# Kernel tuning notes

Hardware: AMD Instinct MI355X
Metric: run time of the kernel (lower is better)

The kernel has to match this reference:

```python
import jax, jax.numpy as jnp
import numpy as np

NEG_SLOPE = 0.2


def setup_inputs() -> dict:
    key = jax.random.key(0)
    k1, k2, k3 = jax.random.split(key, 3)
    bs, n_agents, input_dim = 32, 512, 128
    n_heads, hidden_dim = 8, 64
    h = jax.random.normal(k1, (bs, n_agents, input_dim), dtype=jnp.float32)
    # Linear(input_dim, n_heads*hidden_dim, bias=False), stored as [in, out]
    W = jax.random.normal(k2, (input_dim, n_heads * hidden_dim), dtype=jnp.float32) * (1.0 / np.sqrt(input_dim))
    # xavier_uniform with gain=1.414 on shape (1, n_heads, 2*hidden_dim)
    fan = n_heads + 2 * hidden_dim
    bound = 1.414 * np.sqrt(6.0 / fan)
    att_a = jax.random.uniform(k3, (1, n_heads, 2 * hidden_dim), dtype=jnp.float32,
                               minval=-bound, maxval=bound)
    return {"h": h, "W": W, "att_a": att_a}


def reference(h, W, att_a):
    bs, n_agents, _ = h.shape
    n_heads = att_a.shape[1]
    hidden_dim = att_a.shape[2] // 2
    # h_prime: [bs, n_heads, n_agents, hidden_dim]
    h_prime = (h @ W).reshape(bs, n_agents, n_heads, hidden_dim).transpose(0, 2, 1, 3)
    # Additive score decomposes exactly: (a1.h_i + a2.h_j) == sum(cat(h_i,h_j)*a)
    a_src = att_a[0, :, :hidden_dim]   # [n_heads, hidden_dim]
    a_dst = att_a[0, :, hidden_dim:]   # [n_heads, hidden_dim]
    e_src = jnp.einsum('bhnd,hd->bhn', h_prime, a_src)  # score contribution of node i (row)
    e_dst = jnp.einsum('bhnd,hd->bhn', h_prime, a_dst)  # contribution of node j (col)
    e = e_src[:, :, :, None] + e_dst[:, :, None, :]     # [bs, n_heads, n, n]
    e = jnp.where(e >= 0, e, NEG_SLOPE * e)             # leaky_relu(0.2)
    attention = jax.nn.softmax(e, axis=-1)
    h_new = jnp.einsum('bhnm,bhmd->bhnd', attention, h_prime)
    return jax.nn.elu(h_new)
```

## Files before the change

kernel.cpp:

```cpp
#include <hip/hip_runtime.h>

#define BS 32
#define NA 512
#define ID 128
#define NH 8
#define HD 64
#define NHD 512
#define NEG 0.2f
#define NC 32
#define CH 16

__global__ __launch_bounds__(256) void k1_gemm(
    const float* __restrict__ h, const float* __restrict__ W,
    const float* __restrict__ att, float* __restrict__ hp,
    float* __restrict__ s_out, float* __restrict__ t_out) {
  int blk = blockIdx.x;
  int b = blk >> 5;
  int n0 = (blk & 31) * 16;
  int t = threadIdx.x;
  int lane = t & 63, w = t >> 6;
  int r0 = __builtin_amdgcn_readfirstlane((w >> 1) * 8);
  int chalf = __builtin_amdgcn_readfirstlane(w & 1);
  int col = chalf * 256 + lane * 4;
  int head = col >> 6;
  int d0 = col & 63;
  const float* arow = h + ((size_t)b * NA + n0 + r0) * ID;
  const float* wptr = W + col;

  float4 a0c = {0,0,0,0}, a1c = {0,0,0,0}, a2c = {0,0,0,0}, a3c = {0,0,0,0};
  float4 a4c = {0,0,0,0}, a5c = {0,0,0,0}, a6c = {0,0,0,0}, a7c = {0,0,0,0};

#define K1_ROW(I, C, KK)                                                      \
  { float a_ = arow[(I) * ID + kc + (KK)];                                    \
    C.x += a_ * wv.x; C.y += a_ * wv.y; C.z += a_ * wv.z; C.w += a_ * wv.w; }
  #pragma unroll 1
  for (int kc = 0; kc < ID; kc += 8) {
    #pragma unroll
    for (int kk = 0; kk < 8; ++kk) {
      float4 wv = *(const float4*)(wptr + (size_t)(kc + kk) * NHD);
      K1_ROW(0, a0c, kk) K1_ROW(1, a1c, kk) K1_ROW(2, a2c, kk)
      K1_ROW(3, a3c, kk) K1_ROW(4, a4c, kk) K1_ROW(5, a5c, kk)
      K1_ROW(6, a6c, kk) K1_ROW(7, a7c, kk)
    }
  }
#undef K1_ROW
  {
    size_t off = ((((size_t)b * NH + head) * NA) + (n0 + r0)) * HD + d0;
    *(float4*)(hp + off) = a0c; off += HD;
    *(float4*)(hp + off) = a1c; off += HD;
    *(float4*)(hp + off) = a2c; off += HD;
    *(float4*)(hp + off) = a3c; off += HD;
    *(float4*)(hp + off) = a4c; off += HD;
    *(float4*)(hp + off) = a5c; off += HD;
    *(float4*)(hp + off) = a6c; off += HD;
    *(float4*)(hp + off) = a7c;
  }
  {
    float4 as4 = *(const float4*)(att + head * 128 + d0);
    float4 ad4 = *(const float4*)(att + head * 128 + 64 + d0);
#define DOT4(C, A) ((C).x*(A).x + (C).y*(A).y + (C).z*(A).z + (C).w*(A).w)
    float sp0 = DOT4(a0c, as4), tp0 = DOT4(a0c, ad4);
    float sp1 = DOT4(a1c, as4), tp1 = DOT4(a1c, ad4);
    float sp2 = DOT4(a2c, as4), tp2 = DOT4(a2c, ad4);
    float sp3 = DOT4(a3c, as4), tp3 = DOT4(a3c, ad4);
    float sp4 = DOT4(a4c, as4), tp4 = DOT4(a4c, ad4);
    float sp5 = DOT4(a5c, as4), tp5 = DOT4(a5c, ad4);
    float sp6 = DOT4(a6c, as4), tp6 = DOT4(a6c, ad4);
    float sp7 = DOT4(a7c, as4), tp7 = DOT4(a7c, ad4);
#undef DOT4
    #pragma unroll
    for (int m = 1; m < 16; m <<= 1) {
      sp0 += __shfl_xor(sp0, m, 64); tp0 += __shfl_xor(tp0, m, 64);
      sp1 += __shfl_xor(sp1, m, 64); tp1 += __shfl_xor(tp1, m, 64);
      sp2 += __shfl_xor(sp2, m, 64); tp2 += __shfl_xor(tp2, m, 64);
      sp3 += __shfl_xor(sp3, m, 64); tp3 += __shfl_xor(tp3, m, 64);
      sp4 += __shfl_xor(sp4, m, 64); tp4 += __shfl_xor(tp4, m, 64);
      sp5 += __shfl_xor(sp5, m, 64); tp5 += __shfl_xor(tp5, m, 64);
      sp6 += __shfl_xor(sp6, m, 64); tp6 += __shfl_xor(tp6, m, 64);
      sp7 += __shfl_xor(sp7, m, 64); tp7 += __shfl_xor(tp7, m, 64);
    }
    int g16 = lane & 15;
    int rsel = g16 & 7;
    float sv_ = rsel == 0 ? sp0 : rsel == 1 ? sp1 : rsel == 2 ? sp2 :
                rsel == 3 ? sp3 : rsel == 4 ? sp4 : rsel == 5 ? sp5 :
                rsel == 6 ? sp6 : sp7;
    float tv_ = rsel == 0 ? tp0 : rsel == 1 ? tp1 : rsel == 2 ? tp2 :
                rsel == 3 ? tp3 : rsel == 4 ? tp4 : rsel == 5 ? tp5 :
                rsel == 6 ? tp6 : tp7;
    size_t off = (((size_t)b * NH + head) * NA) + n0 + r0 + rsel;
    if (g16 < 8) s_out[off] = sv_;
    else         t_out[off] = tv_;
  }
}

__global__ __launch_bounds__(512) void k2_fused(
    const float* __restrict__ hp, const float* __restrict__ s_g,
    const float* __restrict__ t_g, float* __restrict__ out) {
  __shared__ float tv[NA]; __shared__ int tpm[NA];
  __shared__ float sv[NA]; __shared__ int spm[NA];
  __shared__ float wp[NA]; __shared__ float wn[NA];
  __shared__ float localP[8 * 64]; __shared__ float localN[8 * 64];
  __shared__ float seedP[8 * 64];  __shared__ float seedN[8 * 64];
  __shared__ float totP[64];
  __shared__ float zps[NA + 1]; __shared__ float znp[NA + 1];
  __shared__ float szP[NC]; __shared__ float szN[NC];
  __shared__ float sufZ[NC + 1]; __shared__ float preZ[NC + 1];
  __shared__ float aA[NA]; __shared__ float aB[NA]; __shared__ float aI[NA];
  __shared__ int aJ[NA]; __shared__ int aR[NA];

  int bh = blockIdx.x;
  int t = threadIdx.x;
  int lane = t & 63, w = t >> 6;
  const float* vbase = hp + (size_t)bh * NA * HD;

  float tvr = t_g[(size_t)bh * NA + t]; int tir = t;
  float svr = s_g[(size_t)bh * NA + t]; int sir = t;
  for (int size = 2; size <= NA; size <<= 1) {
    bool dirAsc = ((t & size) == 0);
    for (int stride = size >> 1; stride > 0; stride >>= 1) {
      float ptv, psv; int pti, psi;
      if (stride >= 64) {
        tv[t] = tvr; tpm[t] = tir; sv[t] = svr; spm[t] = sir;
        __syncthreads();
        ptv = tv[t ^ stride]; pti = tpm[t ^ stride];
        psv = sv[t ^ stride]; psi = spm[t ^ stride];
        __syncthreads();
      } else {
        ptv = __shfl_xor(tvr, stride, 64); pti = __shfl_xor(tir, stride, 64);
        psv = __shfl_xor(svr, stride, 64); psi = __shfl_xor(sir, stride, 64);
      }
      bool mn = (((t & stride) == 0) == dirAsc);
      bool swt = mn ? (ptv < tvr) : (ptv > tvr);
      if (swt) { tvr = ptv; tir = pti; }
      bool sws = mn ? (psv > svr) : (psv < svr);
      if (sws) { svr = psv; sir = psi; }
    }
  }
  tv[t] = tvr; tpm[t] = tir; sv[t] = svr; spm[t] = sir;
  __syncthreads();

  float cmax = fmaxf(tv[NA - 1], 0.f);
  float amax = fmaxf(sv[0], 0.f);
  wp[t] = __expf(tv[t] - cmax);
  wn[t] = __expf(NEG * tv[t] - cmax);
  __syncthreads();

  if (t < 32) {
    float a = 0.f;
    for (int j = t * CH; j < t * CH + CH; ++j) a += wp[j];
    szP[t] = a;
  } else if (t < 64) {
    int c = t - 32; float a = 0.f;
    for (int j = c * CH; j < c * CH + CH; ++j) a += wn[j];
    szN[c] = a;
  }
  {
    float aP = 0.f, aN = 0.f;
    int jb = w * 64;
    for (int jj = 0; jj < 64; ++jj) {
      int j = jb + jj;
      float vv = vbase[(size_t)tpm[j] * HD + lane];
      aP += wp[j] * vv;
      aN += wn[j] * vv;
    }
    localP[w * 64 + lane] = aP;
    localN[w * 64 + lane] = aN;
  }
  __syncthreads();

  if (t == 0) {
    float run = 0.f; sufZ[NC] = 0.f;
    for (int cc = NC - 1; cc >= 0; --cc) { run += szP[cc]; sufZ[cc] = run; }
  } else if (t == 1) {
    float run = 0.f;
    for (int cc = 0; cc <= NC; ++cc) { preZ[cc] = run; if (cc < NC) run += szN[cc]; }
  } else if (t >= 64 && t < 128) {
    int d = t - 64;
    float run = 0.f;
    for (int u = 0; u < 8; ++u) { seedP[u * 64 + d] = run; run += localP[u * 64 + d]; }
    totP[d] = run;
    float run2 = 0.f;
    for (int u = 0; u < 8; ++u) { seedN[u * 64 + d] = run2; run2 += localN[u * 64 + d]; }
  }
  __syncthreads();

  {
    int ch = t >> 4;
    float a = 0.f;
    for (int k = t; k < ch * CH + CH; ++k) a += wp[k];
    zps[t] = a + sufZ[ch + 1];
    float b2 = 0.f;
    for (int k = ch * CH; k < t; ++k) b2 += wn[k];
    znp[t] = preZ[ch] + b2;
    if (t == 0) { zps[NA] = 0.f; znp[NA] = preZ[NC]; }
  }
  __syncthreads();

  {
    float sval = sv[t];
    float A = __expf(sval - amax);
    float B = __expf(NEG * sval - amax);
    float key = -sval;
    int lo = 0, hi = NA;
    while (lo < hi) { int mid = (lo + hi) >> 1; if (tv[mid] < key) lo = mid + 1; else hi = mid; }
    float den = A * zps[lo] + B * znp[lo];
    aA[t] = A; aB[t] = B; aI[t] = 1.f / den; aJ[t] = lo; aR[t] = spm[t];
  }
  __syncthreads();

  {
    int jlo = w * 64, jhi = jlo + 64;
    int p;
    { int lo = 0, hi = NA;
      while (lo < hi) { int mid = (lo + hi) >> 1; if (aJ[mid] < jlo) lo = mid + 1; else hi = mid; }
      p = lo; }
    float prePr = seedP[w * 64 + lane];
    float preNr = seedN[w * 64 + lane];
    float totPd = totP[lane];
    for (int j = jlo; j < jhi; ++j) {
      while (p < NA && aJ[p] == j) {
        float A = aA[p], B = aB[p], inv = aI[p]; int row = aR[p];
        float x = (A * (totPd - prePr) + B * preNr) * inv;
        out[((size_t)bh * NA + row) * HD + lane] = x > 0.f ? x : __expf(x) - 1.f;
        ++p;
      }
      float vv = vbase[(size_t)tpm[j] * HD + lane];
      prePr += wp[j] * vv;
      preNr += wn[j] * vv;
    }
    if (w == 7) {
      while (p < NA) {
        float A = aA[p], B = aB[p], inv = aI[p]; int row = aR[p];
        float x = (A * (totPd - prePr) + B * preNr) * inv;
        out[((size_t)bh * NA + row) * HD + lane] = x > 0.f ? x : __expf(x) - 1.f;
        ++p;
      }
    }
  }
}

extern "C" void kernel_launch(void* const* d_in, const int* in_sizes, int n_in,
                              void* d_out, int out_size, void* d_ws, size_t ws_size,
                              hipStream_t stream) {
  const float* h  = (const float*)d_in[0];
  const float* W  = (const float*)d_in[1];
  const float* att = (const float*)d_in[2];
  float* out = (float*)d_out;
  float* hp    = (float*)d_ws;
  float* s_arr = hp + (size_t)BS * NH * NA * HD;
  float* t_arr = s_arr + (size_t)BS * NH * NA;

  k1_gemm <<<dim3(1024), dim3(256), 0, stream>>>(h, W, att, hp, s_arr, t_arr);
  k2_fused<<<dim3(256),  dim3(512), 0, stream>>>(hp, s_arr, t_arr, out);
}
```

Measured before the change: 157.4 us.

## Stage weighted values in LDS and compute rows directly via chunk prefix sums

The attention kernel now sorts only the destination scores. It gathers the weighted value rows once into a 128KB LDS buffer and builds per-chunk prefix sums over 32 chunks. Each output row is then finished with a 16-element partial sum over its boundary chunk, replacing the sorted-source sweep with its serialized while-loop and second global gather. The source max is taken with a wave reduction instead of a second sort. The large LDS footprint limits residency to one block per CU, and each row now does redundant inner-chunk work.

```diff
diff --git a/kernel.cpp b/kernel.cpp
--- a/kernel.cpp
+++ b/kernel.cpp
@@ -7,8 +7,6 @@
 #define HD 64
 #define NHD 512
 #define NEG 0.2f
-#define NC 32
-#define CH 16
 
 __global__ __launch_bounds__(256) void k1_gemm(
     const float* __restrict__ h, const float* __restrict__ W,
@@ -93,148 +91,163 @@
   }
 }
 
-__global__ __launch_bounds__(512) void k2_fused(
+__global__ __launch_bounds__(512) void k2_lds(
     const float* __restrict__ hp, const float* __restrict__ s_g,
     const float* __restrict__ t_g, float* __restrict__ out) {
-  __shared__ float tv[NA]; __shared__ int tpm[NA];
-  __shared__ float sv[NA]; __shared__ int spm[NA];
-  __shared__ float wp[NA]; __shared__ float wn[NA];
-  __shared__ float localP[8 * 64]; __shared__ float localN[8 * 64];
-  __shared__ float seedP[8 * 64];  __shared__ float seedN[8 * 64];
+  __shared__ float Vp[NA * HD];
+  __shared__ float tvs[NA];
+  __shared__ int   tpm[NA];
+  __shared__ float rr[NA];
+  __shared__ float preP[33 * 64];
+  __shared__ float preN[33 * 64];
   __shared__ float totP[64];
-  __shared__ float zps[NA + 1]; __shared__ float znp[NA + 1];
-  __shared__ float szP[NC]; __shared__ float szN[NC];
-  __shared__ float sufZ[NC + 1]; __shared__ float preZ[NC + 1];
-  __shared__ float aA[NA]; __shared__ float aB[NA]; __shared__ float aI[NA];
-  __shared__ int aJ[NA]; __shared__ int aR[NA];
+  __shared__ float svx[NA];
+  __shared__ float aI[NA];
+  __shared__ int   aJ[NA];
+  __shared__ float szPs[33];
+  __shared__ float szNp[33];
+  __shared__ float smax8[8];
 
   int bh = blockIdx.x;
   int t = threadIdx.x;
   int lane = t & 63, w = t >> 6;
   const float* vbase = hp + (size_t)bh * NA * HD;
 
-  float tvr = t_g[(size_t)bh * NA + t]; int tir = t;
-  float svr = s_g[(size_t)bh * NA + t]; int sir = t;
+  float tvr = t_g[(size_t)bh * NA + t];
+  int tir = t;
   for (int size = 2; size <= NA; size <<= 1) {
     bool dirAsc = ((t & size) == 0);
     for (int stride = size >> 1; stride > 0; stride >>= 1) {
-      float ptv, psv; int pti, psi;
+      float pv; int pi;
       if (stride >= 64) {
-        tv[t] = tvr; tpm[t] = tir; sv[t] = svr; spm[t] = sir;
+        tvs[t] = tvr; tpm[t] = tir;
         __syncthreads();
-        ptv = tv[t ^ stride]; pti = tpm[t ^ stride];
-        psv = sv[t ^ stride]; psi = spm[t ^ stride];
+        pv = tvs[t ^ stride]; pi = tpm[t ^ stride];
         __syncthreads();
       } else {
-        ptv = __shfl_xor(tvr, stride, 64); pti = __shfl_xor(tir, stride, 64);
-        psv = __shfl_xor(svr, stride, 64); psi = __shfl_xor(sir, stride, 64);
+        pv = __shfl_xor(tvr, stride, 64);
+        pi = __shfl_xor(tir, stride, 64);
       }
       bool mn = (((t & stride) == 0) == dirAsc);
-      bool swt = mn ? (ptv < tvr) : (ptv > tvr);
-      if (swt) { tvr = ptv; tir = pti; }
-      bool sws = mn ? (psv > svr) : (psv < svr);
-      if (sws) { svr = psv; sir = psi; }
-    }
-  }
-  tv[t] = tvr; tpm[t] = tir; sv[t] = svr; spm[t] = sir;
-  __syncthreads();
-
-  float cmax = fmaxf(tv[NA - 1], 0.f);
-  float amax = fmaxf(sv[0], 0.f);
-  wp[t] = __expf(tv[t] - cmax);
-  wn[t] = __expf(NEG * tv[t] - cmax);
-  __syncthreads();
-
+      bool sw = mn ? (pv < tvr) : (pv > tvr);
+      if (sw) { tvr = pv; tir = pi; }
+    }
+  }
+  tvs[t] = tvr; tpm[t] = tir;
+  rr[t] = __expf(-0.8f * tvr);
+  float sval = s_g[(size_t)bh * NA + t];
+  svx[t] = sval;
+  {
+    float m = sval;
+    #pragma unroll
+    for (int d = 32; d; d >>= 1) m = fmaxf(m, __shfl_xor(m, d, 64));
+    if (lane == 0) smax8[w] = m;
+  }
+  __syncthreads();
+
+  float cmax = fmaxf(tvs[NA - 1], 0.f);
+  float amax = fmaxf(fmaxf(fmaxf(smax8[0], smax8[1]), fmaxf(smax8[2], smax8[3])),
+                     fmaxf(fmaxf(smax8[4], smax8[5]), fmaxf(smax8[6], smax8[7])));
+  amax = fmaxf(amax, 0.f);
+
+  #pragma unroll 4
+  for (int i = 0; i < 64; ++i) {
+    int j = w * 64 + i;
+    int src = tpm[j];
+    float wpj = __expf(tvs[j] - cmax);
+    Vp[j * HD + lane] = wpj * vbase[(size_t)src * HD + lane];
+  }
+  __syncthreads();
+
+  for (int cc = w; cc < 32; cc += 8) {
+    float aP = 0.f, aN = 0.f;
+    #pragma unroll
+    for (int jj = 0; jj < 16; ++jj) {
+      int j = cc * 16 + jj;
+      float v = Vp[j * HD + lane];
+      aP += v;
+      aN += rr[j] * v;
+    }
+    preP[cc * 64 + lane] = aP;
+    preN[cc * 64 + lane] = aN;
+  }
   if (t < 32) {
     float a = 0.f;
-    for (int j = t * CH; j < t * CH + CH; ++j) a += wp[j];
-    szP[t] = a;
+    for (int j = t * 16; j < t * 16 + 16; ++j) a += __expf(tvs[j] - cmax);
+    szPs[t] = a;
   } else if (t < 64) {
     int c = t - 32; float a = 0.f;
-    for (int j = c * CH; j < c * CH + CH; ++j) a += wn[j];
-    szN[c] = a;
-  }
-  {
-    float aP = 0.f, aN = 0.f;
-    int jb = w * 64;
-    for (int jj = 0; jj < 64; ++jj) {
-      int j = jb + jj;
-      float vv = vbase[(size_t)tpm[j] * HD + lane];
-      aP += wp[j] * vv;
-      aN += wn[j] * vv;
-    }
-    localP[w * 64 + lane] = aP;
-    localN[w * 64 + lane] = aN;
+    for (int j = c * 16; j < c * 16 + 16; ++j) a += __expf(NEG * tvs[j] - cmax);
+    szNp[c] = a;
   }
   __syncthreads();
 
   if (t == 0) {
-    float run = 0.f; sufZ[NC] = 0.f;
-    for (int cc = NC - 1; cc >= 0; --cc) { run += szP[cc]; sufZ[cc] = run; }
+    float run = 0.f;
+    szPs[32] = 0.f;
+    for (int cc = 31; cc >= 0; --cc) { float o = szPs[cc]; szPs[cc] = run + o; run += o; }
   } else if (t == 1) {
     float run = 0.f;
-    for (int cc = 0; cc <= NC; ++cc) { preZ[cc] = run; if (cc < NC) run += szN[cc]; }
+    for (int cc = 0; cc < 32; ++cc) { float o = szNp[cc]; szNp[cc] = run; run += o; }
+    szNp[32] = run;
   } else if (t >= 64 && t < 128) {
-    int d = t - 64;
-    float run = 0.f;
-    for (int u = 0; u < 8; ++u) { seedP[u * 64 + d] = run; run += localP[u * 64 + d]; }
+    int d = t - 64; float run = 0.f;
+    for (int cc = 0; cc < 32; ++cc) {
+      float o = preP[cc * 64 + d]; preP[cc * 64 + d] = run; run += o;
+    }
+    preP[32 * 64 + d] = run;
     totP[d] = run;
-    float run2 = 0.f;
-    for (int u = 0; u < 8; ++u) { seedN[u * 64 + d] = run2; run2 += localN[u * 64 + d]; }
-  }
-  __syncthreads();
-
-  {
-    int ch = t >> 4;
-    float a = 0.f;
-    for (int k = t; k < ch * CH + CH; ++k) a += wp[k];
-    zps[t] = a + sufZ[ch + 1];
-    float b2 = 0.f;
-    for (int k = ch * CH; k < t; ++k) b2 += wn[k];
-    znp[t] = preZ[ch] + b2;
-    if (t == 0) { zps[NA] = 0.f; znp[NA] = preZ[NC]; }
-  }
-  __syncthreads();
-
-  {
-    float sval = sv[t];
+  } else if (t >= 128 && t < 192) {
+    int d = t - 128; float run = 0.f;
+    for (int cc = 0; cc < 32; ++cc) {
+      float o = preN[cc * 64 + d]; preN[cc * 64 + d] = run; run += o;
+    }
+    preN[32 * 64 + d] = run;
+  }
+  __syncthreads();
+
+  {
     float A = __expf(sval - amax);
     float B = __expf(NEG * sval - amax);
     float key = -sval;
     int lo = 0, hi = NA;
-    while (lo < hi) { int mid = (lo + hi) >> 1; if (tv[mid] < key) lo = mid + 1; else hi = mid; }
-    float den = A * zps[lo] + B * znp[lo];
-    aA[t] = A; aB[t] = B; aI[t] = 1.f / den; aJ[t] = lo; aR[t] = spm[t];
-  }
-  __syncthreads();
-
-  {
-    int jlo = w * 64, jhi = jlo + 64;
-    int p;
-    { int lo = 0, hi = NA;
-      while (lo < hi) { int mid = (lo + hi) >> 1; if (aJ[mid] < jlo) lo = mid + 1; else hi = mid; }
-      p = lo; }
-    float prePr = seedP[w * 64 + lane];
-    float preNr = seedN[w * 64 + lane];
-    float totPd = totP[lane];
-    for (int j = jlo; j < jhi; ++j) {
-      while (p < NA && aJ[p] == j) {
-        float A = aA[p], B = aB[p], inv = aI[p]; int row = aR[p];
-        float x = (A * (totPd - prePr) + B * preNr) * inv;
-        out[((size_t)bh * NA + row) * HD + lane] = x > 0.f ? x : __expf(x) - 1.f;
-        ++p;
+    while (lo < hi) { int mid = (lo + hi) >> 1; if (tvs[mid] < key) lo = mid + 1; else hi = mid; }
+    int js = lo;
+    float zps, znp;
+    if (js == NA) {
+      zps = 0.f; znp = szNp[32];
+    } else {
+      int ch = js >> 4;
+      zps = szPs[ch + 1];
+      for (int k = js; k < ch * 16 + 16; ++k) zps += __expf(tvs[k] - cmax);
+      znp = szNp[ch];
+      for (int k = ch * 16; k < js; ++k) znp += __expf(NEG * tvs[k] - cmax);
+    }
+    aI[t] = 1.f / (A * zps + B * znp);
+    aJ[t] = js;
+  }
+  __syncthreads();
+
+  {
+    for (int i = 0; i < 64; ++i) {
+      int row = w * 64 + i;
+      int js = aJ[row];
+      float inv = aI[row];
+      float s = svx[row];
+      float A = __expf(s - amax);
+      float B = __expf(NEG * s - amax);
+      int cs = js >> 4; if (cs > 31) cs = 31;
+      float pos = totP[lane] - preP[(cs + 1) * 64 + lane];
+      float neg = preN[cs * 64 + lane];
+      #pragma unroll
+      for (int jj = 0; jj < 16; ++jj) {
+        int j = cs * 16 + jj;
+        float v = Vp[j * HD + lane];
+        if (j >= js) pos += v;
+        else         neg += rr[j] * v;
       }
-      float vv = vbase[(size_t)tpm[j] * HD + lane];
-      prePr += wp[j] * vv;
-      preNr += wn[j] * vv;
-    }
-    if (w == 7) {
-      while (p < NA) {
-        float A = aA[p], B = aB[p], inv = aI[p]; int row = aR[p];
-        float x = (A * (totPd - prePr) + B * preNr) * inv;
-        out[((size_t)bh * NA + row) * HD + lane] = x > 0.f ? x : __expf(x) - 1.f;
-        ++p;
-      }
+      float x = (A * pos + B * neg) * inv;
+      out[((size_t)bh * NA + row) * HD + lane] = x > 0.f ? x : __expf(x) - 1.f;
     }
   }
 }
@@ -250,6 +263,6 @@
   float* s_arr = hp + (size_t)BS * NH * NA * HD;
   float* t_arr = s_arr + (size_t)BS * NH * NA;
 
-  k1_gemm <<<dim3(1024), dim3(256), 0, stream>>>(h, W, att, hp, s_arr, t_arr);
-  k2_fused<<<dim3(256),  dim3(512), 0, stream>>>(hp, s_arr, t_arr, out);
+  k1_gemm<<<dim3(1024), dim3(256), 0, stream>>>(h, W, att, hp, s_arr, t_arr);
+  k2_lds <<<dim3(256),  dim3(512), 0, stream>>>(hp, s_arr, t_arr, out);
 }
```

Result: slower. 188.4 us (+19.7%).

## Split attention apply into table-build and gather kernels, enlarge GEMM row tile

Applied to the files above, without the earlier changes.

The fused second kernel is split in two. The first writes full per-position suffix/prefix weighted-sum tables and per-row scaling info to global memory. A new highly parallel kernel then gathers one table row per output row and applies the ELU, which replaces the serial per-warp row emission that had load imbalance. The source-score sort is replaced by a max reduction, and the GEMM kernel now computes 16 rows per warp with float4 loads along k. This costs extra global traffic, roughly two tables of 32 MB each written and then read, plus one more launch.

```diff
diff --git a/kernel.cpp b/kernel.cpp
--- a/kernel.cpp
+++ b/kernel.cpp
@@ -9,17 +9,18 @@
 #define NEG 0.2f
 #define NC 32
 #define CH 16
+#define TROWS (NA + 1)
 
 __global__ __launch_bounds__(256) void k1_gemm(
     const float* __restrict__ h, const float* __restrict__ W,
     const float* __restrict__ att, float* __restrict__ hp,
     float* __restrict__ s_out, float* __restrict__ t_out) {
   int blk = blockIdx.x;
-  int b = blk >> 5;
-  int n0 = (blk & 31) * 16;
+  int b = blk >> 4;
+  int n0 = (blk & 15) * 32;
   int t = threadIdx.x;
   int lane = t & 63, w = t >> 6;
-  int r0 = __builtin_amdgcn_readfirstlane((w >> 1) * 8);
+  int r0 = __builtin_amdgcn_readfirstlane((w >> 1) * 16);
   int chalf = __builtin_amdgcn_readfirstlane(w & 1);
   int col = chalf * 256 + lane * 4;
   int head = col >> 6;
@@ -27,124 +28,142 @@
   const float* arow = h + ((size_t)b * NA + n0 + r0) * ID;
   const float* wptr = W + col;
 
-  float4 a0c = {0,0,0,0}, a1c = {0,0,0,0}, a2c = {0,0,0,0}, a3c = {0,0,0,0};
-  float4 a4c = {0,0,0,0}, a5c = {0,0,0,0}, a6c = {0,0,0,0}, a7c = {0,0,0,0};
-
-#define K1_ROW(I, C, KK)                                                      \
-  { float a_ = arow[(I) * ID + kc + (KK)];                                    \
-    C.x += a_ * wv.x; C.y += a_ * wv.y; C.z += a_ * wv.z; C.w += a_ * wv.w; }
+  float4 c0 = {0,0,0,0}, c1 = {0,0,0,0}, c2 = {0,0,0,0}, c3 = {0,0,0,0};
+  float4 c4 = {0,0,0,0}, c5 = {0,0,0,0}, c6 = {0,0,0,0}, c7 = {0,0,0,0};
+  float4 c8 = {0,0,0,0}, c9 = {0,0,0,0}, cA = {0,0,0,0}, cB = {0,0,0,0};
+  float4 cC = {0,0,0,0}, cD = {0,0,0,0}, cE = {0,0,0,0}, cF = {0,0,0,0};
+
+#define K1_ROW(I, C)                                                          \
+  { float4 av = *(const float4*)(arow + (I) * ID + kc);                       \
+    C.x += av.x*wv0.x + av.y*wv1.x + av.z*wv2.x + av.w*wv3.x;                 \
+    C.y += av.x*wv0.y + av.y*wv1.y + av.z*wv2.y + av.w*wv3.y;                 \
+    C.z += av.x*wv0.z + av.y*wv1.z + av.z*wv2.z + av.w*wv3.z;                 \
+    C.w += av.x*wv0.w + av.y*wv1.w + av.z*wv2.w + av.w*wv3.w; }
   #pragma unroll 1
-  for (int kc = 0; kc < ID; kc += 8) {
-    #pragma unroll
-    for (int kk = 0; kk < 8; ++kk) {
-      float4 wv = *(const float4*)(wptr + (size_t)(kc + kk) * NHD);
-      K1_ROW(0, a0c, kk) K1_ROW(1, a1c, kk) K1_ROW(2, a2c, kk)
-      K1_ROW(3, a3c, kk) K1_ROW(4, a4c, kk) K1_ROW(5, a5c, kk)
-      K1_ROW(6, a6c, kk) K1_ROW(7, a7c, kk)
-    }
+  for (int kc = 0; kc < ID; kc += 4) {
+    float4 wv0 = *(const float4*)(wptr + (size_t)(kc + 0) * NHD);
+    float4 wv1 = *(const float4*)(wptr + (size_t)(kc + 1) * NHD);
+    float4 wv2 = *(const float4*)(wptr + (size_t)(kc + 2) * NHD);
+    float4 wv3 = *(const float4*)(wptr + (size_t)(kc + 3) * NHD);
+    K1_ROW( 0, c0) K1_ROW( 1, c1) K1_ROW( 2, c2) K1_ROW( 3, c3)
+    K1_ROW( 4, c4) K1_ROW( 5, c5) K1_ROW( 6, c6) K1_ROW( 7, c7)
+    K1_ROW( 8, c8) K1_ROW( 9, c9) K1_ROW(10, cA) K1_ROW(11, cB)
+    K1_ROW(12, cC) K1_ROW(13, cD) K1_ROW(14, cE) K1_ROW(15, cF)
   }
 #undef K1_ROW
   {
     size_t off = ((((size_t)b * NH + head) * NA) + (n0 + r0)) * HD + d0;
-    *(float4*)(hp + off) = a0c; off += HD;
-    *(float4*)(hp + off) = a1c; off += HD;
-    *(float4*)(hp + off) = a2c; off += HD;
-    *(float4*)(hp + off) = a3c; off += HD;
-    *(float4*)(hp + off) = a4c; off += HD;
-    *(float4*)(hp + off) = a5c; off += HD;
-    *(float4*)(hp + off) = a6c; off += HD;
-    *(float4*)(hp + off) = a7c;
+    *(float4*)(hp + off) = c0; off += HD; *(float4*)(hp + off) = c1; off += HD;
+    *(float4*)(hp + off) = c2; off += HD; *(float4*)(hp + off) = c3; off += HD;
+    *(float4*)(hp + off) = c4; off += HD; *(float4*)(hp + off) = c5; off += HD;
+    *(float4*)(hp + off) = c6; off += HD; *(float4*)(hp + off) = c7; off += HD;
+    *(float4*)(hp + off) = c8; off += HD; *(float4*)(hp + off) = c9; off += HD;
+    *(float4*)(hp + off) = cA; off += HD; *(float4*)(hp + off) = cB; off += HD;
+    *(float4*)(hp + off) = cC; off += HD; *(float4*)(hp + off) = cD; off += HD;
+    *(float4*)(hp + off) = cE; off += HD; *(float4*)(hp + off) = cF;
   }
   {
     float4 as4 = *(const float4*)(att + head * 128 + d0);
     float4 ad4 = *(const float4*)(att + head * 128 + 64 + d0);
 #define DOT4(C, A) ((C).x*(A).x + (C).y*(A).y + (C).z*(A).z + (C).w*(A).w)
-    float sp0 = DOT4(a0c, as4), tp0 = DOT4(a0c, ad4);
-    float sp1 = DOT4(a1c, as4), tp1 = DOT4(a1c, ad4);
-    float sp2 = DOT4(a2c, as4), tp2 = DOT4(a2c, ad4);
-    float sp3 = DOT4(a3c, as4), tp3 = DOT4(a3c, ad4);
-    float sp4 = DOT4(a4c, as4), tp4 = DOT4(a4c, ad4);
-    float sp5 = DOT4(a5c, as4), tp5 = DOT4(a5c, ad4);
-    float sp6 = DOT4(a6c, as4), tp6 = DOT4(a6c, ad4);
-    float sp7 = DOT4(a7c, as4), tp7 = DOT4(a7c, ad4);
+    float sp[16], tp[16];
+    sp[ 0]=DOT4(c0,as4); tp[ 0]=DOT4(c0,ad4); sp[ 1]=DOT4(c1,as4); tp[ 1]=DOT4(c1,ad4);
+    sp[ 2]=DOT4(c2,as4); tp[ 2]=DOT4(c2,ad4); sp[ 3]=DOT4(c3,as4); tp[ 3]=DOT4(c3,ad4);
+    sp[ 4]=DOT4(c4,as4); tp[ 4]=DOT4(c4,ad4); sp[ 5]=DOT4(c5,as4); tp[ 5]=DOT4(c5,ad4);
+    sp[ 6]=DOT4(c6,as4); tp[ 6]=DOT4(c6,ad4); sp[ 7]=DOT4(c7,as4); tp[ 7]=DOT4(c7,ad4);
+    sp[ 8]=DOT4(c8,as4); tp[ 8]=DOT4(c8,ad4); sp[ 9]=DOT4(c9,as4); tp[ 9]=DOT4(c9,ad4);
+    sp[10]=DOT4(cA,as4); tp[10]=DOT4(cA,ad4); sp[11]=DOT4(cB,as4); tp[11]=DOT4(cB,ad4);
+    sp[12]=DOT4(cC,as4); tp[12]=DOT4(cC,ad4); sp[13]=DOT4(cD,as4); tp[13]=DOT4(cD,ad4);
+    sp[14]=DOT4(cE,as4); tp[14]=DOT4(cE,ad4); sp[15]=DOT4(cF,as4); tp[15]=DOT4(cF,ad4);
 #undef DOT4
     #pragma unroll
     for (int m = 1; m < 16; m <<= 1) {
-      sp0 += __shfl_xor(sp0, m, 64); tp0 += __shfl_xor(tp0, m, 64);
-      sp1 += __shfl_xor(sp1, m, 64); tp1 += __shfl_xor(tp1, m, 64);
-      sp2 += __shfl_xor(sp2, m, 64); tp2 += __shfl_xor(tp2, m, 64);
-      sp3 += __shfl_xor(sp3, m, 64); tp3 += __shfl_xor(tp3, m, 64);
-      sp4 += __shfl_xor(sp4, m, 64); tp4 += __shfl_xor(tp4, m, 64);
-      sp5 += __shfl_xor(sp5, m, 64); tp5 += __shfl_xor(tp5, m, 64);
-      sp6 += __shfl_xor(sp6, m, 64); tp6 += __shfl_xor(tp6, m, 64);
-      sp7 += __shfl_xor(sp7, m, 64); tp7 += __shfl_xor(tp7, m, 64);
+      #pragma unroll
+      for (int i = 0; i < 16; ++i) {
+        sp[i] += __shfl_xor(sp[i], m, 64);
+        tp[i] += __shfl_xor(tp[i], m, 64);
+      }
     }
     int g16 = lane & 15;
-    int rsel = g16 & 7;
-    float sv_ = rsel == 0 ? sp0 : rsel == 1 ? sp1 : rsel == 2 ? sp2 :
-                rsel == 3 ? sp3 : rsel == 4 ? sp4 : rsel == 5 ? sp5 :
-                rsel == 6 ? sp6 : sp7;
-    float tv_ = rsel == 0 ? tp0 : rsel == 1 ? tp1 : rsel == 2 ? tp2 :
-                rsel == 3 ? tp3 : rsel == 4 ? tp4 : rsel == 5 ? tp5 :
-                rsel == 6 ? tp6 : tp7;
-    size_t off = (((size_t)b * NH + head) * NA) + n0 + r0 + rsel;
-    if (g16 < 8) s_out[off] = sv_;
-    else         t_out[off] = tv_;
-  }
-}
-
-__global__ __launch_bounds__(512) void k2_fused(
+    float sv_ = sp[0], tv_ = tp[0];
+    #pragma unroll
+    for (int i = 1; i < 16; ++i) if (g16 == i) { sv_ = sp[i]; tv_ = tp[i]; }
+    size_t off = (((size_t)b * NH + head) * NA) + n0 + r0 + g16;
+    s_out[off] = sv_;
+    t_out[off] = tv_;
+  }
+}
+
+__global__ __launch_bounds__(512) void k2a_tables(
     const float* __restrict__ hp, const float* __restrict__ s_g,
-    const float* __restrict__ t_g, float* __restrict__ out) {
+    const float* __restrict__ t_g, float* __restrict__ sufPfull,
+    float* __restrict__ preNfull, float4* __restrict__ rinfo_g) {
   __shared__ float tv[NA]; __shared__ int tpm[NA];
-  __shared__ float sv[NA]; __shared__ int spm[NA];
   __shared__ float wp[NA]; __shared__ float wn[NA];
   __shared__ float localP[8 * 64]; __shared__ float localN[8 * 64];
   __shared__ float seedP[8 * 64];  __shared__ float seedN[8 * 64];
-  __shared__ float totP[64];
+  __shared__ float totP[64]; __shared__ float totN[64];
   __shared__ float zps[NA + 1]; __shared__ float znp[NA + 1];
   __shared__ float szP[NC]; __shared__ float szN[NC];
   __shared__ float sufZ[NC + 1]; __shared__ float preZ[NC + 1];
-  __shared__ float aA[NA]; __shared__ float aB[NA]; __shared__ float aI[NA];
-  __shared__ int aJ[NA]; __shared__ int aR[NA];
+  __shared__ float smax8[8];
 
   int bh = blockIdx.x;
   int t = threadIdx.x;
   int lane = t & 63, w = t >> 6;
   const float* vbase = hp + (size_t)bh * NA * HD;
 
-  float tvr = t_g[(size_t)bh * NA + t]; int tir = t;
-  float svr = s_g[(size_t)bh * NA + t]; int sir = t;
+  float tvr = t_g[(size_t)bh * NA + t];
+  int tir = t;
   for (int size = 2; size <= NA; size <<= 1) {
     bool dirAsc = ((t & size) == 0);
     for (int stride = size >> 1; stride > 0; stride >>= 1) {
-      float ptv, psv; int pti, psi;
+      float pv; int pi;
       if (stride >= 64) {
-        tv[t] = tvr; tpm[t] = tir; sv[t] = svr; spm[t] = sir;
+        tv[t] = tvr; tpm[t] = tir;
         __syncthreads();
-        ptv = tv[t ^ stride]; pti = tpm[t ^ stride];
-        psv = sv[t ^ stride]; psi = spm[t ^ stride];
+        pv = tv[t ^ stride]; pi = tpm[t ^ stride];
         __syncthreads();
       } else {
-        ptv = __shfl_xor(tvr, stride, 64); pti = __shfl_xor(tir, stride, 64);
-        psv = __shfl_xor(svr, stride, 64); psi = __shfl_xor(sir, stride, 64);
+        pv = __shfl_xor(tvr, stride, 64);
+        pi = __shfl_xor(tir, stride, 64);
       }
       bool mn = (((t & stride) == 0) == dirAsc);
-      bool swt = mn ? (ptv < tvr) : (ptv > tvr);
-      if (swt) { tvr = ptv; tir = pti; }
-      bool sws = mn ? (psv > svr) : (psv < svr);
-      if (sws) { svr = psv; sir = psi; }
-    }
-  }
-  tv[t] = tvr; tpm[t] = tir; sv[t] = svr; spm[t] = sir;
+      bool sw = mn ? (pv < tvr) : (pv > tvr);
+      if (sw) { tvr = pv; tir = pi; }
+    }
+  }
+  tv[t] = tvr; tpm[t] = tir;
+  float sval = s_g[(size_t)bh * NA + t];
+  {
+    float m = sval;
+    #pragma unroll
+    for (int d = 32; d; d >>= 1) m = fmaxf(m, __shfl_xor(m, d, 64));
+    if (lane == 0) smax8[w] = m;
+  }
   __syncthreads();
 
   float cmax = fmaxf(tv[NA - 1], 0.f);
-  float amax = fmaxf(sv[0], 0.f);
+  float amax = fmaxf(fmaxf(fmaxf(smax8[0], smax8[1]), fmaxf(smax8[2], smax8[3])),
+                     fmaxf(fmaxf(smax8[4], smax8[5]), fmaxf(smax8[6], smax8[7])));
+  amax = fmaxf(amax, 0.f);
   wp[t] = __expf(tv[t] - cmax);
   wn[t] = __expf(NEG * tv[t] - cmax);
   __syncthreads();
 
+  {
+    float aP = 0.f, aN = 0.f;
+    int jb = w * 64;
+    #pragma unroll 4
+    for (int jj = 0; jj < 64; ++jj) {
+      int j = jb + jj;
+      float vv = vbase[(size_t)tpm[j] * HD + lane];
+      aP += wp[j] * vv;
+      aN += wn[j] * vv;
+    }
+    localP[w * 64 + lane] = aP;
+    localN[w * 64 + lane] = aN;
+  }
   if (t < 32) {
     float a = 0.f;
     for (int j = t * CH; j < t * CH + CH; ++j) a += wp[j];
@@ -154,18 +173,6 @@
     for (int j = c * CH; j < c * CH + CH; ++j) a += wn[j];
     szN[c] = a;
   }
-  {
-    float aP = 0.f, aN = 0.f;
-    int jb = w * 64;
-    for (int jj = 0; jj < 64; ++jj) {
-      int j = jb + jj;
-      float vv = vbase[(size_t)tpm[j] * HD + lane];
-      aP += wp[j] * vv;
-      aN += wn[j] * vv;
-    }
-    localP[w * 64 + lane] = aP;
-    localN[w * 64 + lane] = aN;
-  }
   __syncthreads();
 
   if (t == 0) {
@@ -175,12 +182,13 @@
     float run = 0.f;
     for (int cc = 0; cc <= NC; ++cc) { preZ[cc] = run; if (cc < NC) run += szN[cc]; }
   } else if (t >= 64 && t < 128) {
-    int d = t - 64;
-    float run = 0.f;
+    int d = t - 64; float run = 0.f;
     for (int u = 0; u < 8; ++u) { seedP[u * 64 + d] = run; run += localP[u * 64 + d]; }
     totP[d] = run;
-    float run2 = 0.f;
-    for (int u = 0; u < 8; ++u) { seedN[u * 64 + d] = run2; run2 += localN[u * 64 + d]; }
+  } else if (t >= 128 && t < 192) {
+    int d = t - 128; float run = 0.f;
+    for (int u = 0; u < 8; ++u) { seedN[u * 64 + d] = run; run += localN[u * 64 + d]; }
+    totN[d] = run;
   }
   __syncthreads();
 
@@ -197,46 +205,53 @@
   __syncthreads();
 
   {
-    float sval = sv[t];
+    float* sP = sufPfull + (size_t)bh * TROWS * 64;
+    float* pN = preNfull + (size_t)bh * TROWS * 64;
+    int jb = w * 64;
+    float runP = seedP[w * 64 + lane];
+    float runN = seedN[w * 64 + lane];
+    float totPd = totP[lane];
+    #pragma unroll 4
+    for (int jj = 0; jj < 64; ++jj) {
+      int j = jb + jj;
+      sP[(size_t)j * 64 + lane] = totPd - runP;
+      pN[(size_t)j * 64 + lane] = runN;
+      float vv = vbase[(size_t)tpm[j] * HD + lane];
+      runP += wp[j] * vv;
+      runN += wn[j] * vv;
+    }
+    if (t < 64) {
+      sP[(size_t)NA * 64 + t] = 0.f;
+      pN[(size_t)NA * 64 + t] = totN[t];
+    }
+  }
+
+  {
     float A = __expf(sval - amax);
     float B = __expf(NEG * sval - amax);
     float key = -sval;
     int lo = 0, hi = NA;
     while (lo < hi) { int mid = (lo + hi) >> 1; if (tv[mid] < key) lo = mid + 1; else hi = mid; }
-    float den = A * zps[lo] + B * znp[lo];
-    aA[t] = A; aB[t] = B; aI[t] = 1.f / den; aJ[t] = lo; aR[t] = spm[t];
-  }
-  __syncthreads();
-
-  {
-    int jlo = w * 64, jhi = jlo + 64;
-    int p;
-    { int lo = 0, hi = NA;
-      while (lo < hi) { int mid = (lo + hi) >> 1; if (aJ[mid] < jlo) lo = mid + 1; else hi = mid; }
-      p = lo; }
-    float prePr = seedP[w * 64 + lane];
-    float preNr = seedN[w * 64 + lane];
-    float totPd = totP[lane];
-    for (int j = jlo; j < jhi; ++j) {
-      while (p < NA && aJ[p] == j) {
-        float A = aA[p], B = aB[p], inv = aI[p]; int row = aR[p];
-        float x = (A * (totPd - prePr) + B * preNr) * inv;
-        out[((size_t)bh * NA + row) * HD + lane] = x > 0.f ? x : __expf(x) - 1.f;
-        ++p;
-      }
-      float vv = vbase[(size_t)tpm[j] * HD + lane];
-      prePr += wp[j] * vv;
-      preNr += wn[j] * vv;
-    }
-    if (w == 7) {
-      while (p < NA) {
-        float A = aA[p], B = aB[p], inv = aI[p]; int row = aR[p];
-        float x = (A * (totPd - prePr) + B * preNr) * inv;
-        out[((size_t)bh * NA + row) * HD + lane] = x > 0.f ? x : __expf(x) - 1.f;
-        ++p;
-      }
-    }
-  }
+    int js = lo;
+    float den = A * zps[js] + B * znp[js];
+    float4 ri;
+    ri.x = A; ri.y = B; ri.z = 1.f / den; ri.w = __int_as_float(js);
+    rinfo_g[(size_t)bh * NA + t] = ri;
+  }
+}
+
+__global__ __launch_bounds__(256) void k2b_apply(
+    const float* __restrict__ sufPfull, const float* __restrict__ preNfull,
+    const float4* __restrict__ rinfo_g, float* __restrict__ out) {
+  int blk = blockIdx.x;
+  int bh = blk >> 7;
+  int row = (blk & 127) * 4 + (threadIdx.x >> 6);
+  int lane = threadIdx.x & 63;
+  float4 ri = rinfo_g[(size_t)bh * NA + row];
+  int js = __float_as_int(ri.w);
+  size_t tb = ((size_t)bh * TROWS + js) * 64 + lane;
+  float x = (ri.x * sufPfull[tb] + ri.y * preNfull[tb]) * ri.z;
+  out[(((size_t)bh * NA) + row) * 64 + lane] = x > 0.f ? x : __expf(x) - 1.f;
 }
 
 extern "C" void kernel_launch(void* const* d_in, const int* in_sizes, int n_in,
@@ -249,7 +264,13 @@
   float* hp    = (float*)d_ws;
   float* s_arr = hp + (size_t)BS * NH * NA * HD;
   float* t_arr = s_arr + (size_t)BS * NH * NA;
-
-  k1_gemm <<<dim3(1024), dim3(256), 0, stream>>>(h, W, att, hp, s_arr, t_arr);
-  k2_fused<<<dim3(256),  dim3(512), 0, stream>>>(hp, s_arr, t_arr, out);
-}
+  float* sufPf = t_arr + (size_t)BS * NH * NA;
+  float* preNf = sufPf + (size_t)BS * NH * TROWS * 64;
+  float* rinfo = preNf + (size_t)BS * NH * TROWS * 64;
+
+  k1_gemm   <<<dim3(512),   dim3(256), 0, stream>>>(h, W, att, hp, s_arr, t_arr);
+  k2a_tables<<<dim3(256),   dim3(512), 0, stream>>>(hp, s_arr, t_arr, sufPf,
+                                                    preNf, (float4*)rinfo);
+  k2b_apply <<<dim3(32768), dim3(256), 0, stream>>>(sufPf, preNf,
+                                                    (float4*)rinfo, out);
+}
```

Result: slower. 204.1 us (+29.6%).

## Split fused attention kernel into prefix-table build and parallel apply kernels

Applied to the files above, without the earlier changes.

Splits the second kernel into one that sorts only the column scores and materializes per-bucket prefix sums of the weighted values to global memory, and a highly parallel kernel that computes each output row from one table lookup. It drops the sort of row scores, replacing it with a wave max reduction, and removes the serial per-wave merge loop. In exchange it writes and reads a large intermediate table through global memory and adds a launch.

```diff
diff --git a/kernel.cpp b/kernel.cpp
--- a/kernel.cpp
+++ b/kernel.cpp
@@ -9,6 +9,7 @@
 #define NEG 0.2f
 #define NC 32
 #define CH 16
+#define TROWS (NA + 1)
 
 __global__ __launch_bounds__(256) void k1_gemm(
     const float* __restrict__ h, const float* __restrict__ W,
@@ -93,58 +94,76 @@
   }
 }
 
-__global__ __launch_bounds__(512) void k2_fused(
+__global__ __launch_bounds__(512) void k2a_tables(
     const float* __restrict__ hp, const float* __restrict__ s_g,
-    const float* __restrict__ t_g, float* __restrict__ out) {
+    const float* __restrict__ t_g, float2* __restrict__ tab,
+    float4* __restrict__ rinfo_g) {
   __shared__ float tv[NA]; __shared__ int tpm[NA];
-  __shared__ float sv[NA]; __shared__ int spm[NA];
   __shared__ float wp[NA]; __shared__ float wn[NA];
   __shared__ float localP[8 * 64]; __shared__ float localN[8 * 64];
   __shared__ float seedP[8 * 64];  __shared__ float seedN[8 * 64];
-  __shared__ float totP[64];
+  __shared__ float totP[64]; __shared__ float totN[64];
   __shared__ float zps[NA + 1]; __shared__ float znp[NA + 1];
   __shared__ float szP[NC]; __shared__ float szN[NC];
   __shared__ float sufZ[NC + 1]; __shared__ float preZ[NC + 1];
-  __shared__ float aA[NA]; __shared__ float aB[NA]; __shared__ float aI[NA];
-  __shared__ int aJ[NA]; __shared__ int aR[NA];
+  __shared__ float smax8[8];
 
   int bh = blockIdx.x;
   int t = threadIdx.x;
   int lane = t & 63, w = t >> 6;
   const float* vbase = hp + (size_t)bh * NA * HD;
 
-  float tvr = t_g[(size_t)bh * NA + t]; int tir = t;
-  float svr = s_g[(size_t)bh * NA + t]; int sir = t;
+  float tvr = t_g[(size_t)bh * NA + t];
+  int tir = t;
   for (int size = 2; size <= NA; size <<= 1) {
     bool dirAsc = ((t & size) == 0);
     for (int stride = size >> 1; stride > 0; stride >>= 1) {
-      float ptv, psv; int pti, psi;
+      float pv; int pi;
       if (stride >= 64) {
-        tv[t] = tvr; tpm[t] = tir; sv[t] = svr; spm[t] = sir;
+        tv[t] = tvr; tpm[t] = tir;
         __syncthreads();
-        ptv = tv[t ^ stride]; pti = tpm[t ^ stride];
-        psv = sv[t ^ stride]; psi = spm[t ^ stride];
+        pv = tv[t ^ stride]; pi = tpm[t ^ stride];
         __syncthreads();
       } else {
-        ptv = __shfl_xor(tvr, stride, 64); pti = __shfl_xor(tir, stride, 64);
-        psv = __shfl_xor(svr, stride, 64); psi = __shfl_xor(sir, stride, 64);
+        pv = __shfl_xor(tvr, stride, 64);
+        pi = __shfl_xor(tir, stride, 64);
       }
       bool mn = (((t & stride) == 0) == dirAsc);
-      bool swt = mn ? (ptv < tvr) : (ptv > tvr);
-      if (swt) { tvr = ptv; tir = pti; }
-      bool sws = mn ? (psv > svr) : (psv < svr);
-      if (sws) { svr = psv; sir = psi; }
-    }
-  }
-  tv[t] = tvr; tpm[t] = tir; sv[t] = svr; spm[t] = sir;
+      bool sw = mn ? (pv < tvr) : (pv > tvr);
+      if (sw) { tvr = pv; tir = pi; }
+    }
+  }
+  tv[t] = tvr; tpm[t] = tir;
+  float sval = s_g[(size_t)bh * NA + t];
+  {
+    float m = sval;
+    #pragma unroll
+    for (int d = 32; d; d >>= 1) m = fmaxf(m, __shfl_xor(m, d, 64));
+    if (lane == 0) smax8[w] = m;
+  }
   __syncthreads();
 
   float cmax = fmaxf(tv[NA - 1], 0.f);
-  float amax = fmaxf(sv[0], 0.f);
+  float amax = fmaxf(fmaxf(fmaxf(smax8[0], smax8[1]), fmaxf(smax8[2], smax8[3])),
+                     fmaxf(fmaxf(smax8[4], smax8[5]), fmaxf(smax8[6], smax8[7])));
+  amax = fmaxf(amax, 0.f);
   wp[t] = __expf(tv[t] - cmax);
   wn[t] = __expf(NEG * tv[t] - cmax);
   __syncthreads();
 
+  {
+    float aP = 0.f, aN = 0.f;
+    int jb = w * 64;
+    #pragma unroll 16
+    for (int jj = 0; jj < 64; ++jj) {
+      int j = jb + jj;
+      float vv = vbase[(size_t)tpm[j] * HD + lane];
+      aP += wp[j] * vv;
+      aN += wn[j] * vv;
+    }
+    localP[w * 64 + lane] = aP;
+    localN[w * 64 + lane] = aN;
+  }
   if (t < 32) {
     float a = 0.f;
     for (int j = t * CH; j < t * CH + CH; ++j) a += wp[j];
@@ -154,18 +173,6 @@
     for (int j = c * CH; j < c * CH + CH; ++j) a += wn[j];
     szN[c] = a;
   }
-  {
-    float aP = 0.f, aN = 0.f;
-    int jb = w * 64;
-    for (int jj = 0; jj < 64; ++jj) {
-      int j = jb + jj;
-      float vv = vbase[(size_t)tpm[j] * HD + lane];
-      aP += wp[j] * vv;
-      aN += wn[j] * vv;
-    }
-    localP[w * 64 + lane] = aP;
-    localN[w * 64 + lane] = aN;
-  }
   __syncthreads();
 
   if (t == 0) {
@@ -175,12 +182,13 @@
     float run = 0.f;
     for (int cc = 0; cc <= NC; ++cc) { preZ[cc] = run; if (cc < NC) run += szN[cc]; }
   } else if (t >= 64 && t < 128) {
-    int d = t - 64;
-    float run = 0.f;
+    int d = t - 64; float run = 0.f;
     for (int u = 0; u < 8; ++u) { seedP[u * 64 + d] = run; run += localP[u * 64 + d]; }
     totP[d] = run;
-    float run2 = 0.f;
-    for (int u = 0; u < 8; ++u) { seedN[u * 64 + d] = run2; run2 += localN[u * 64 + d]; }
+  } else if (t >= 128 && t < 192) {
+    int d = t - 128; float run = 0.f;
+    for (int u = 0; u < 8; ++u) { seedN[u * 64 + d] = run; run += localN[u * 64 + d]; }
+    totN[d] = run;
   }
   __syncthreads();
 
@@ -197,46 +205,52 @@
   __syncthreads();
 
   {
-    float sval = sv[t];
+    float2* tb2 = tab + (size_t)bh * TROWS * 64;
+    int jb = w * 64;
+    float runP = seedP[w * 64 + lane];
+    float runN = seedN[w * 64 + lane];
+    float totPd = totP[lane];
+    #pragma unroll 16
+    for (int jj = 0; jj < 64; ++jj) {
+      int j = jb + jj;
+      float2 e; e.x = totPd - runP; e.y = runN;
+      tb2[(size_t)j * 64 + lane] = e;
+      float vv = vbase[(size_t)tpm[j] * HD + lane];
+      runP += wp[j] * vv;
+      runN += wn[j] * vv;
+    }
+    if (t < 64) {
+      float2 e; e.x = 0.f; e.y = totN[t];
+      tb2[(size_t)NA * 64 + t] = e;
+    }
+  }
+
+  {
     float A = __expf(sval - amax);
     float B = __expf(NEG * sval - amax);
     float key = -sval;
     int lo = 0, hi = NA;
     while (lo < hi) { int mid = (lo + hi) >> 1; if (tv[mid] < key) lo = mid + 1; else hi = mid; }
-    float den = A * zps[lo] + B * znp[lo];
-    aA[t] = A; aB[t] = B; aI[t] = 1.f / den; aJ[t] = lo; aR[t] = spm[t];
-  }
-  __syncthreads();
-
-  {
-    int jlo = w * 64, jhi = jlo + 64;
-    int p;
-    { int lo = 0, hi = NA;
-      while (lo < hi) { int mid = (lo + hi) >> 1; if (aJ[mid] < jlo) lo = mid + 1; else hi = mid; }
-      p = lo; }
-    float prePr = seedP[w * 64 + lane];
-    float preNr = seedN[w * 64 + lane];
-    float totPd = totP[lane];
-    for (int j = jlo; j < jhi; ++j) {
-      while (p < NA && aJ[p] == j) {
-        float A = aA[p], B = aB[p], inv = aI[p]; int row = aR[p];
-        float x = (A * (totPd - prePr) + B * preNr) * inv;
-        out[((size_t)bh * NA + row) * HD + lane] = x > 0.f ? x : __expf(x) - 1.f;
-        ++p;
-      }
-      float vv = vbase[(size_t)tpm[j] * HD + lane];
-      prePr += wp[j] * vv;
-      preNr += wn[j] * vv;
-    }
-    if (w == 7) {
-      while (p < NA) {
-        float A = aA[p], B = aB[p], inv = aI[p]; int row = aR[p];
-        float x = (A * (totPd - prePr) + B * preNr) * inv;
-        out[((size_t)bh * NA + row) * HD + lane] = x > 0.f ? x : __expf(x) - 1.f;
-        ++p;
-      }
-    }
-  }
+    int js = lo;
+    float den = A * zps[js] + B * znp[js];
+    float4 ri;
+    ri.x = A; ri.y = B; ri.z = 1.f / den; ri.w = __int_as_float(js);
+    rinfo_g[(size_t)bh * NA + t] = ri;
+  }
+}
+
+__global__ __launch_bounds__(256) void k2b_apply(
+    const float2* __restrict__ tab, const float4* __restrict__ rinfo_g,
+    float* __restrict__ out) {
+  int blk = blockIdx.x;
+  int bh = blk >> 7;
+  int row = (blk & 127) * 4 + (threadIdx.x >> 6);
+  int lane = threadIdx.x & 63;
+  float4 ri = rinfo_g[(size_t)bh * NA + row];
+  int js = __float_as_int(ri.w);
+  float2 pv = tab[((size_t)bh * TROWS + js) * 64 + lane];
+  float x = (ri.x * pv.x + ri.y * pv.y) * ri.z;
+  out[(((size_t)bh * NA) + row) * 64 + lane] = x > 0.f ? x : __expf(x) - 1.f;
 }
 
 extern "C" void kernel_launch(void* const* d_in, const int* in_sizes, int n_in,
@@ -249,7 +263,12 @@
   float* hp    = (float*)d_ws;
   float* s_arr = hp + (size_t)BS * NH * NA * HD;
   float* t_arr = s_arr + (size_t)BS * NH * NA;
-
-  k1_gemm <<<dim3(1024), dim3(256), 0, stream>>>(h, W, att, hp, s_arr, t_arr);
-  k2_fused<<<dim3(256),  dim3(512), 0, stream>>>(hp, s_arr, t_arr, out);
-}
+  float* tabf  = t_arr + (size_t)BS * NH * NA;
+  float* rinfo = tabf + (size_t)BS * NH * TROWS * 64 * 2;
+
+  k1_gemm   <<<dim3(1024),  dim3(256), 0, stream>>>(h, W, att, hp, s_arr, t_arr);
+  k2a_tables<<<dim3(256),   dim3(512), 0, stream>>>(hp, s_arr, t_arr,
+                                                    (float2*)tabf, (float4*)rinfo);
+  k2b_apply <<<dim3(32768), dim3(256), 0, stream>>>((float2*)tabf,
+                                                    (float4*)rinfo, out);
+}
```

Result: slower. 165.6 us (+5.2%).
